# Performance work log

Measured on AMD Instinct MI355X. Metric: run time of the kernel, lower is better.

## Reference

```python
import jax, jax.numpy as jnp
import numpy as np

B, L, C = 256, 16384, 4
DMICE_P = 0.1
IGNORE = 3  # padding class, also ignore_index for CE


def setup_inputs() -> dict:
    key = jax.random.key(0)
    k1, k2, k3 = jax.random.split(key, 3)
    pred = jax.random.normal(k1, (B, C, L), dtype=jnp.float32)
    # real labels in {0,1,2}; tail after a random length is padded with 3
    base = jax.random.randint(k2, (B, L), 0, 3, dtype=jnp.int32)
    lengths = jax.random.randint(k3, (B,), L // 2, L, dtype=jnp.int32)
    valid = jnp.arange(L, dtype=jnp.int32)[None, :] < lengths[:, None]
    labels = jnp.where(valid, base, IGNORE)
    return {"pred": pred, "labels": labels}


def reference(pred, labels):
    # pred: [B, C=4, L] logits; labels: [B, L] int in {0,1,2,3}, 3 = pad/ignore
    b, c, l = pred.shape
    f32 = pred.dtype

    # --- CrossEntropyLoss(ignore_index=3), mean over valid tokens ---
    valid = (labels != IGNORE)
    logp = jax.nn.log_softmax(pred, axis=1)                         # [B,4,L]
    picked = jnp.take_along_axis(logp, labels[:, None, :], axis=1)[:, 0, :]  # [B,L]
    ce = -(picked * valid.astype(f32)).sum() / valid.sum().astype(f32)

    # --- per-sample ragged prefix length j (first label==3, else L-1) ---
    is_pad = (labels == IGNORE)
    has_pad = jnp.any(is_pad, axis=1)
    j = jnp.where(has_pad, jnp.argmax(is_pad, axis=1), l - 1)        # [B]
    mask = (jnp.arange(l)[None, :] < j[:, None]).astype(f32)         # [B,L]

    # --- DMI: mat = onehot(labels)^T @ softmax(pred[:, :3]) / j ---
    probs = jax.nn.softmax(pred[:, :3, :], axis=1)                   # [B,3,L]
    onehot = jax.nn.one_hot(labels, 3, dtype=f32) * mask[..., None]  # [B,L,3]
    mat = jnp.einsum('blc,bdl->bcd', onehot, probs) / j[:, None, None].astype(f32)  # [B,3,3]
    det = jnp.linalg.det(mat)                                        # [B]
    dmi = jnp.where(det < 0,
                    jnp.log(jnp.abs(det) + 1e-3),
                    -jnp.log(jnp.abs(det) + 1e-3))
    loss = DMICE_P * (dmi.sum() / b) + ce
    return loss
```

## Files before the change

### kernel.cpp

```cpp
#include <hip/hip_runtime.h>
#include <math.h>

constexpr int B_ = 256;
constexpr int L_ = 16384;
constexpr int C_ = 4;
constexpr int CHUNKS = 4;
constexpr int CHUNK = L_ / CHUNKS;
constexpr int THREADS = 256;
constexpr int NVAL = 11;
constexpr int PSTRIDE = 12;

__global__ __launch_bounds__(THREADS) void dmice_partial(
    const float* __restrict__ pred, const int* __restrict__ labels,
    float* __restrict__ partial) {
  const int blk = blockIdx.x;
  const int b = blk >> 2;
  const int ch = blk & (CHUNKS - 1);

  const float* p0 = pred + (size_t)b * (C_ * L_) + (size_t)ch * CHUNK;
  const float* p1 = p0 + L_;
  const float* p2 = p0 + 2 * L_;
  const float* p3 = p0 + 3 * L_;
  const int* lb = labels + (size_t)b * L_ + (size_t)ch * CHUNK;
  const int t = threadIdx.x;

  float ce = 0.f, cnt = 0.f;
  float m00 = 0.f, m01 = 0.f, m02 = 0.f;
  float m10 = 0.f, m11 = 0.f, m12 = 0.f;
  float m20 = 0.f, m21 = 0.f, m22 = 0.f;

  auto proc = [&](float v0, float v1, float v2, float v3, int lab) {
    float mx = fmaxf(fmaxf(v0, v1), fmaxf(v2, v3));
    float e0 = __expf(v0 - mx);
    float e1 = __expf(v1 - mx);
    float e2 = __expf(v2 - mx);
    float e3 = __expf(v3 - mx);
    float s3 = e0 + e1 + e2;
    float s4 = s3 + e3;
    if (lab != 3) {
      float xl = (lab == 0) ? v0 : ((lab == 1) ? v1 : v2);
      ce += (mx + __logf(s4)) - xl;
      cnt += 1.f;
      float inv = 1.f / s3;
      float q0 = e0 * inv, q1 = e1 * inv, q2 = e2 * inv;
      bool c0 = (lab == 0), c1 = (lab == 1), c2 = (lab == 2);
      m00 += c0 ? q0 : 0.f; m01 += c0 ? q1 : 0.f; m02 += c0 ? q2 : 0.f;
      m10 += c1 ? q0 : 0.f; m11 += c1 ? q1 : 0.f; m12 += c1 ? q2 : 0.f;
      m20 += c2 ? q0 : 0.f; m21 += c2 ? q1 : 0.f; m22 += c2 ? q2 : 0.f;
    }
  };

  constexpr int ITERS = CHUNK / (THREADS * 4);
#pragma unroll
  for (int it = 0; it < ITERS; ++it) {
    const int idx = (it * THREADS + t) * 4;
    float4 x0 = *(const float4*)(p0 + idx);
    float4 x1 = *(const float4*)(p1 + idx);
    float4 x2 = *(const float4*)(p2 + idx);
    float4 x3 = *(const float4*)(p3 + idx);
    int4 lv = *(const int4*)(lb + idx);
    proc(x0.x, x1.x, x2.x, x3.x, lv.x);
    proc(x0.y, x1.y, x2.y, x3.y, lv.y);
    proc(x0.z, x1.z, x2.z, x3.z, lv.z);
    proc(x0.w, x1.w, x2.w, x3.w, lv.w);
  }

  float vals[NVAL] = {ce, cnt, m00, m01, m02, m10, m11, m12, m20, m21, m22};
#pragma unroll
  for (int off = 32; off > 0; off >>= 1) {
#pragma unroll
    for (int k = 0; k < NVAL; ++k) vals[k] += __shfl_down(vals[k], off, 64);
  }
  __shared__ float red[THREADS / 64][NVAL];
  const int wave = t >> 6, lane = t & 63;
  if (lane == 0) {
#pragma unroll
    for (int k = 0; k < NVAL; ++k) red[wave][k] = vals[k];
  }
  __syncthreads();
  if (t == 0) {
#pragma unroll
    for (int k = 0; k < NVAL; ++k) {
      float s = red[0][k] + red[1][k] + red[2][k] + red[3][k];
      partial[(size_t)blk * PSTRIDE + k] = s;
    }
  }
}

__global__ __launch_bounds__(THREADS) void dmice_final(
    const float* __restrict__ partial, float* __restrict__ out) {
  const int b = threadIdx.x;
  float v[NVAL];
#pragma unroll
  for (int k = 0; k < NVAL; ++k) v[k] = 0.f;
  for (int c = 0; c < CHUNKS; ++c) {
    const float* p = partial + (size_t)(b * CHUNKS + c) * PSTRIDE;
#pragma unroll
    for (int k = 0; k < NVAL; ++k) v[k] += p[k];
  }
  float ce = v[0], cnt = v[1];
  float inv = 1.f / cnt;
  float a00 = v[2] * inv, a01 = v[3] * inv, a02 = v[4] * inv;
  float a10 = v[5] * inv, a11 = v[6] * inv, a12 = v[7] * inv;
  float a20 = v[8] * inv, a21 = v[9] * inv, a22 = v[10] * inv;
  float det = a00 * (a11 * a22 - a12 * a21)
            - a01 * (a10 * a22 - a12 * a20)
            + a02 * (a10 * a21 - a11 * a20);
  float lg = __logf(fabsf(det) + 1e-3f);
  float dmi = (det < 0.f) ? lg : -lg;

  float r[3] = {dmi, ce, cnt};
#pragma unroll
  for (int off = 32; off > 0; off >>= 1) {
#pragma unroll
    for (int k = 0; k < 3; ++k) r[k] += __shfl_down(r[k], off, 64);
  }
  __shared__ float red[THREADS / 64][3];
  const int wave = b >> 6, lane = b & 63;
  if (lane == 0) {
#pragma unroll
    for (int k = 0; k < 3; ++k) red[wave][k] = r[k];
  }
  __syncthreads();
  if (b == 0) {
    float dmi_s = red[0][0] + red[1][0] + red[2][0] + red[3][0];
    float ce_s  = red[0][1] + red[1][1] + red[2][1] + red[3][1];
    float cnt_s = red[0][2] + red[1][2] + red[2][2] + red[3][2];
    out[0] = 0.1f * (dmi_s * (1.f / (float)B_)) + ce_s / cnt_s;
  }
}

extern "C" void kernel_launch(void* const* d_in, const int* in_sizes, int n_in,
                              void* d_out, int out_size, void* d_ws, size_t ws_size,
                              hipStream_t stream) {
  const float* pred = (const float*)d_in[0];
  const int* labels = (const int*)d_in[1];
  float* out = (float*)d_out;
  float* partial = (float*)d_ws;

  dmice_partial<<<B_ * CHUNKS, THREADS, 0, stream>>>(pred, labels, partial);
  dmice_final<<<1, THREADS, 0, stream>>>(partial, out);
}
```

Measured before the change: 105.0 us.

## Fuse final reduction into partial kernel via last-block atomic counter

```diff
diff --git a/kernel.cpp b/kernel.cpp
--- a/kernel.cpp
+++ b/kernel.cpp
@@ -4,17 +4,19 @@
 constexpr int B_ = 256;
 constexpr int L_ = 16384;
 constexpr int C_ = 4;
-constexpr int CHUNKS = 4;
+constexpr int CHUNKS = 8;
 constexpr int CHUNK = L_ / CHUNKS;
 constexpr int THREADS = 256;
 constexpr int NVAL = 11;
 constexpr int PSTRIDE = 12;
+constexpr int NBLK = B_ * CHUNKS;
 
-__global__ __launch_bounds__(THREADS) void dmice_partial(
+__global__ __launch_bounds__(THREADS) void dmice_fused(
     const float* __restrict__ pred, const int* __restrict__ labels,
-    float* __restrict__ partial) {
+    float* __restrict__ partial, unsigned int* __restrict__ counter,
+    float* __restrict__ out) {
   const int blk = blockIdx.x;
-  const int b = blk >> 2;
+  const int b = blk >> 3;
   const int ch = blk & (CHUNKS - 1);
 
   const float* p0 = pred + (size_t)b * (C_ * L_) + (size_t)ch * CHUNK;
@@ -42,11 +44,12 @@
       ce += (mx + __logf(s4)) - xl;
       cnt += 1.f;
       float inv = 1.f / s3;
-      float q0 = e0 * inv, q1 = e1 * inv, q2 = e2 * inv;
-      bool c0 = (lab == 0), c1 = (lab == 1), c2 = (lab == 2);
-      m00 += c0 ? q0 : 0.f; m01 += c0 ? q1 : 0.f; m02 += c0 ? q2 : 0.f;
-      m10 += c1 ? q0 : 0.f; m11 += c1 ? q1 : 0.f; m12 += c1 ? q2 : 0.f;
-      m20 += c2 ? q0 : 0.f; m21 += c2 ? q1 : 0.f; m22 += c2 ? q2 : 0.f;
+      float r0 = (lab == 0) ? inv : 0.f;
+      float r1 = (lab == 1) ? inv : 0.f;
+      float r2 = (lab == 2) ? inv : 0.f;
+      m00 = fmaf(e0, r0, m00); m01 = fmaf(e1, r0, m01); m02 = fmaf(e2, r0, m02);
+      m10 = fmaf(e0, r1, m10); m11 = fmaf(e1, r1, m11); m12 = fmaf(e2, r1, m12);
+      m20 = fmaf(e0, r2, m20); m21 = fmaf(e1, r2, m21); m22 = fmaf(e2, r2, m22);
     }
   };
 
@@ -78,28 +81,36 @@
     for (int k = 0; k < NVAL; ++k) red[wave][k] = vals[k];
   }
   __syncthreads();
+
+  __shared__ bool amLast;
   if (t == 0) {
+    float s[NVAL];
 #pragma unroll
-    for (int k = 0; k < NVAL; ++k) {
-      float s = red[0][k] + red[1][k] + red[2][k] + red[3][k];
-      partial[(size_t)blk * PSTRIDE + k] = s;
-    }
+    for (int k = 0; k < NVAL; ++k)
+      s[k] = red[0][k] + red[1][k] + red[2][k] + red[3][k];
+    float* pp = partial + (size_t)blk * PSTRIDE;
+    *(float4*)(pp + 0) = make_float4(s[0], s[1], s[2], s[3]);
+    *(float4*)(pp + 4) = make_float4(s[4], s[5], s[6], s[7]);
+    *(float4*)(pp + 8) = make_float4(s[8], s[9], s[10], 0.f);
+    __threadfence();
+    unsigned int old = atomicAdd(counter, 1u);
+    amLast = (old == (unsigned int)(NBLK - 1));
   }
-}
+  __syncthreads();
+  if (!amLast) return;
+  __threadfence();
 
-__global__ __launch_bounds__(THREADS) void dmice_final(
-    const float* __restrict__ partial, float* __restrict__ out) {
-  const int b = threadIdx.x;
+  const int bb = t;
   float v[NVAL];
 #pragma unroll
   for (int k = 0; k < NVAL; ++k) v[k] = 0.f;
   for (int c = 0; c < CHUNKS; ++c) {
-    const float* p = partial + (size_t)(b * CHUNKS + c) * PSTRIDE;
+    const float* p = partial + (size_t)(bb * CHUNKS + c) * PSTRIDE;
 #pragma unroll
     for (int k = 0; k < NVAL; ++k) v[k] += p[k];
   }
-  float ce = v[0], cnt = v[1];
-  float inv = 1.f / cnt;
+  float ces = v[0], cnts = v[1];
+  float inv = 1.f / cnts;
   float a00 = v[2] * inv, a01 = v[3] * inv, a02 = v[4] * inv;
   float a10 = v[5] * inv, a11 = v[6] * inv, a12 = v[7] * inv;
   float a20 = v[8] * inv, a21 = v[9] * inv, a22 = v[10] * inv;
@@ -109,23 +120,22 @@
   float lg = __logf(fabsf(det) + 1e-3f);
   float dmi = (det < 0.f) ? lg : -lg;
 
-  float r[3] = {dmi, ce, cnt};
+  float r[3] = {dmi, ces, cnts};
 #pragma unroll
   for (int off = 32; off > 0; off >>= 1) {
 #pragma unroll
     for (int k = 0; k < 3; ++k) r[k] += __shfl_down(r[k], off, 64);
   }
-  __shared__ float red[THREADS / 64][3];
-  const int wave = b >> 6, lane = b & 63;
+  __shared__ float red2[THREADS / 64][3];
   if (lane == 0) {
 #pragma unroll
-    for (int k = 0; k < 3; ++k) red[wave][k] = r[k];
+    for (int k = 0; k < 3; ++k) red2[wave][k] = r[k];
   }
   __syncthreads();
-  if (b == 0) {
-    float dmi_s = red[0][0] + red[1][0] + red[2][0] + red[3][0];
-    float ce_s  = red[0][1] + red[1][1] + red[2][1] + red[3][1];
-    float cnt_s = red[0][2] + red[1][2] + red[2][2] + red[3][2];
+  if (t == 0) {
+    float dmi_s = red2[0][0] + red2[1][0] + red2[2][0] + red2[3][0];
+    float ce_s  = red2[0][1] + red2[1][1] + red2[2][1] + red2[3][1];
+    float cnt_s = red2[0][2] + red2[1][2] + red2[2][2] + red2[3][2];
     out[0] = 0.1f * (dmi_s * (1.f / (float)B_)) + ce_s / cnt_s;
   }
 }
@@ -137,7 +147,8 @@
   const int* labels = (const int*)d_in[1];
   float* out = (float*)d_out;
   float* partial = (float*)d_ws;
+  unsigned int* counter = (unsigned int*)((char*)d_ws + NBLK * PSTRIDE * sizeof(float));
 
-  dmice_partial<<<B_ * CHUNKS, THREADS, 0, stream>>>(pred, labels, partial);
-  dmice_final<<<1, THREADS, 0, stream>>>(partial, out);
+  hipMemsetAsync(counter, 0, sizeof(unsigned int), stream);
+  dmice_fused<<<NBLK, THREADS, 0, stream>>>(pred, labels, partial, counter, out);
 }
```

Measured after the change: 178.5 us. +70.0%, slower.
